# Kernel tuning notes

Hardware: AMD Instinct MI355X
Metric: run time of the kernel (lower is better)

Reference implementation:

```python
import jax, jax.numpy as jnp
import numpy as np

DIM = 2048
N_HEADS = 16
N_KV_HEADS = 4
HEAD_DIM = DIM // N_HEADS


def setup_inputs() -> dict:
    key = jax.random.key(0)
    k1, k2, k3, k4, k5 = jax.random.split(key, 5)
    B, T = 2, 2048
    scale = 1.0 / np.sqrt(DIM)
    x = jax.random.normal(k1, (B, T, DIM), dtype=jnp.float32)
    # weights stored as [in, out] so forward is x @ W (same math as nn.Linear)
    Wq = jax.random.normal(k2, (DIM, DIM), dtype=jnp.float32) * scale
    Wk = jax.random.normal(k3, (DIM, N_KV_HEADS * HEAD_DIM), dtype=jnp.float32) * scale
    Wv = jax.random.normal(k4, (DIM, N_KV_HEADS * HEAD_DIM), dtype=jnp.float32) * scale
    Wo = jax.random.normal(k5, (DIM, DIM), dtype=jnp.float32) * scale
    return {"x": x, "Wq": Wq, "Wk": Wk, "Wv": Wv, "Wo": Wo}


def reference(x, Wq, Wk, Wv, Wo):
    B, T, C = x.shape
    G = N_HEADS // N_KV_HEADS  # query heads per kv head
    # projections
    q = (x @ Wq).reshape(B, T, N_KV_HEADS, G, HEAD_DIM)   # [B,T,K,G,d]
    k = (x @ Wk).reshape(B, T, N_KV_HEADS, HEAD_DIM)      # [B,T,K,d]
    v = (x @ Wv).reshape(B, T, N_KV_HEADS, HEAD_DIM)      # [B,T,K,d]
    # attention scores: grouped heads share kv head (no repeat_interleave copy)
    att = jnp.einsum('btkgd,bskd->bkgts', q, k) / np.sqrt(HEAD_DIM)  # [B,K,G,T,T]
    att = jax.nn.softmax(att, axis=-1)
    out = jnp.einsum('bkgts,bskd->btkgd', att, v).reshape(B, T, C)
    return out @ Wo
```

## Files before the change

kernel.cpp:

```cpp
#include <hip/hip_runtime.h>
#include <hip/hip_bf16.h>

typedef __hip_bfloat16 bf16;
typedef __attribute__((ext_vector_type(8))) short short8;
typedef __attribute__((ext_vector_type(4))) short short4v;
typedef __attribute__((ext_vector_type(4))) float f32x4;

#define DIMC 2048
#define TSEQ 2048
#define NB 2
#define KVH 4
#define NH 16
#define HD 128
#define KVD 512
#define QSCALE 0.12751744f

#if __has_builtin(__builtin_amdgcn_exp2f)
#define EXP2(x) __builtin_amdgcn_exp2f(x)
#else
#define EXP2(x) exp2f(x)
#endif

__device__ __forceinline__ float fmax3(float a, float b, float c) {
  return fmaxf(fmaxf(a, b), c);
}

__device__ __forceinline__ void mfma16(f32x4& acc, short8 a, short8 b) {
  acc = __builtin_amdgcn_mfma_f32_16x16x32_bf16(a, b, acc, 0, 0, 0);
}

__device__ __forceinline__ void gload_lds16(const bf16* g, bf16* l) {
  __builtin_amdgcn_global_load_lds(
      (const __attribute__((address_space(1))) void*)g,
      (__attribute__((address_space(3))) void*)l, 16, 0, 0);
}

__device__ __forceinline__ int swz(int row, int col) {
  return col ^ ((row & 7) << 3);
}

__global__ __launch_bounds__(256) void transpose_all(const float* __restrict__ Wq,
                                                     const float* __restrict__ Wk,
                                                     const float* __restrict__ Wv,
                                                     const float* __restrict__ Wo,
                                                     const float* __restrict__ x,
                                                     bf16* __restrict__ WT3,
                                                     bf16* __restrict__ WoT,
                                                     bf16* __restrict__ xb) {
  const int y = blockIdx.y;
  if (y >= 80) {
    long base = (((long)(y - 80) * 32 + blockIdx.x) * 2048) + threadIdx.x;
#pragma unroll
    for (int j = 0; j < 8; ++j) {
      long i = base + j * 256;
      const f32x4 v = *(const f32x4*)(x + i * 4);
      union { short4v s; bf16 h[4]; } u;
#pragma unroll
      for (int k = 0; k < 4; ++k) u.h[k] = __float2bfloat16(v[k]);
      *(short4v*)(xb + i * 4) = u.s;
    }
    return;
  }
  __shared__ bf16 tile[64][72];
  const float* in;
  bf16* out;
  int C, rb, cb;
  float scale = 1.0f;
  if (y < 32) {
    in = Wq; out = WT3; C = 2048;
    rb = y * 64; cb = blockIdx.x * 64; scale = QSCALE;
  } else if (y < 40) {
    in = Wk; out = WT3 + (long)2048 * DIMC; C = 512;
    rb = blockIdx.x * 64; cb = (y - 32) * 64;
  } else if (y < 48) {
    in = Wv; out = WT3 + (long)2560 * DIMC; C = 512;
    rb = blockIdx.x * 64; cb = (y - 40) * 64;
  } else {
    in = Wo; out = WoT; C = 2048;
    rb = (y - 48) * 64; cb = blockIdx.x * 64;
  }
  int tx = threadIdx.x & 63, ty = threadIdx.x >> 6;
  for (int i = ty; i < 64; i += 4)
    tile[i][tx] = __float2bfloat16(in[(long)(rb + i) * C + cb + tx] * scale);
  __syncthreads();
  for (int i = ty; i < 64; i += 4)
    out[(long)(cb + i) * DIMC + rb + tx] = tile[tx][i];
}

#define XCD_REMAP(NX)                                                          \
  const int flat_ = blockIdx.y * (NX) + blockIdx.x;                            \
  const int tot_ = (NX) * gridDim.y;                                           \
  const int log_ = (flat_ & 7) * (tot_ >> 3) + (flat_ >> 3);                   \
  const long m0 = (long)(log_ / (NX)) * 128, n0 = (long)(log_ % (NX)) * 128;

#define GEMM_BODY(A_, Bt_, K_)                                                  \
  const int tid = threadIdx.x;                                                  \
  const int lane = tid & 63, wid = tid >> 6;                                    \
  const int wm = (wid >> 1) * 64, wn = (wid & 1) * 64;                          \
  f32x4 acc[4][4] = {};                                                         \
  const int srow = lane >> 2, scol = (lane & 3) * 8;                            \
  const bf16* Ag = A_ + (m0 + srow) * (long)K_ + scol;                          \
  const bf16* Bg = Bt_ + (n0 + srow) * (long)K_ + scol;                         \
  for (int k0 = 0; k0 < K_; k0 += 32) {                                         \
    for (int p = 0; p < 2; ++p) {                                               \
      int rr = p * 64 + wid * 16;                                               \
      gload_lds16(Ag + (long)rr * K_ + k0, As + rr * 32);                       \
      gload_lds16(Bg + (long)rr * K_ + k0, Bs + rr * 32);                       \
    }                                                                           \
    __syncthreads();                                                            \
    const int ko = (lane >> 4) * 8;                                             \
    short8 af[4], bq[4];                                                        \
    _Pragma("unroll") for (int i = 0; i < 4; ++i) {                             \
      af[i] = *(const short8*)(As + (wm + i * 16 + (lane & 15)) * 32 + ko);     \
      bq[i] = *(const short8*)(Bs + (wn + i * 16 + (lane & 15)) * 32 + ko);     \
    }                                                                           \
    _Pragma("unroll") for (int i = 0; i < 4; ++i)                               \
      _Pragma("unroll") for (int j = 0; j < 4; ++j)                             \
        mfma16(acc[i][j], af[i], bq[j]);                                        \
    __syncthreads();                                                            \
  }                                                                             \
  const int cr = (lane >> 4) * 4, cc = lane & 15;

__global__ __launch_bounds__(256) void gemm_qkv(const bf16* __restrict__ A,
                                                const bf16* __restrict__ Bt,
                                                bf16* __restrict__ qp,
                                                bf16* __restrict__ kp,
                                                bf16* __restrict__ vT) {
  __shared__ bf16 As[128 * 32];
  __shared__ bf16 Bs[128 * 32];
  XCD_REMAP(24)
  GEMM_BODY(A, Bt, 2048)
#pragma unroll
  for (int i = 0; i < 4; ++i)
#pragma unroll
    for (int j = 0; j < 4; ++j)
#pragma unroll
      for (int r = 0; r < 4; ++r) {
        long m = m0 + wm + i * 16 + cr + r;
        long n = n0 + wn + j * 16 + cc;
        float val = acc[i][j][r];
        if (n0 < 2048) {
          qp[m * DIMC + n] = __float2bfloat16(val);
        } else if (n0 < 2560) {
          kp[m * KVD + (n - 2048)] = __float2bfloat16(val);
        } else {
          long nn = n - 2560;
          long z = (m >> 11) * 4 + (nn >> 7);
          vT[z * (HD * (long)TSEQ) + (nn & 127) * (long)TSEQ + (m & 2047)] =
              __float2bfloat16(val);
        }
      }
}

__global__ __launch_bounds__(256) void gemm_out(const bf16* __restrict__ A,
                                                const bf16* __restrict__ Bt,
                                                float* __restrict__ C) {
  __shared__ bf16 As[128 * 32];
  __shared__ bf16 Bs[128 * 32];
  XCD_REMAP(16)
  GEMM_BODY(A, Bt, 2048)
#pragma unroll
  for (int i = 0; i < 4; ++i)
#pragma unroll
    for (int j = 0; j < 4; ++j)
#pragma unroll
      for (int r = 0; r < 4; ++r) {
        long m = m0 + wm + i * 16 + cr + r;
        long n = n0 + wn + j * 16 + cc;
        C[m * DIMC + n] = acc[i][j][r];
      }
}

__global__ __launch_bounds__(256, 2) void attn_fwd(const bf16* __restrict__ Qp,
                                                   const bf16* __restrict__ Kp,
                                                   const bf16* __restrict__ Vt,
                                                   bf16* __restrict__ AO) {
  __shared__ bf16 Ks[2][64 * 128];
  __shared__ bf16 Vts[2][128 * 64];
  const int tid = threadIdx.x;
  const int lane = tid & 63, wid = tid >> 6;
  const int h = blockIdx.y, b = blockIdx.z;
  const int kv = h >> 2;
  const int t0 = blockIdx.x * 128;
  const int lr = lane & 15, lg = lane >> 4;

  short8 aq[2][4];
#pragma unroll
  for (int f = 0; f < 2; ++f) {
    const bf16* qrow =
        Qp + ((long)(b * TSEQ + t0 + wid * 32 + f * 16 + lr)) * DIMC + h * HD + lg * 8;
#pragma unroll
    for (int c = 0; c < 4; ++c) aq[f][c] = *(const short8*)(qrow + c * 32);
  }
  f32x4 o[2][8] = {};
  float mrun[2] = {-1e30f, -1e30f}, lrun[2] = {0.f, 0.f};

  const bf16* Kg = Kp + (long)b * TSEQ * KVD + kv * HD;
  const bf16* Vg = Vt + ((long)(b * KVH + kv)) * HD * TSEQ;

  const int krow = tid >> 2;
  const int vrow = tid >> 1;
  short8 kreg[2][2], vreg[2][2];
#pragma unroll
  for (int s = 0; s < 2; ++s)
#pragma unroll
    for (int p = 0; p < 2; ++p) {
      kreg[s][p] = *(const short8*)(Kg + (long)krow * KVD + (2 * (tid & 3) + s) * 16 + p * 8);
      vreg[s][p] = *(const short8*)(Vg + (long)vrow * TSEQ + (2 * (tid & 1) + s) * 16 + 8 * p);
    }

  for (int s0 = 0; s0 < TSEQ; s0 += 64) {
    const int buf = (s0 >> 6) & 1;
    bf16* Kb = Ks[buf];
    bf16* Vb = Vts[buf];
#pragma unroll
    for (int s = 0; s < 2; ++s)
#pragma unroll
      for (int p = 0; p < 2; ++p) {
        int kc0 = (2 * (tid & 3) + s) * 16;
        *(short8*)(Kb + krow * 128 + swz(krow, kc0 + p * 8)) = kreg[s][p];
        int va = 2 * (tid & 1) + s;
        union { short8 v8; short4v q[2]; } u;
        u.v8 = vreg[s][p];
        int sl1 = (4 * (va >> 1) + 2 * p + vrow) & 7;
        int sl2 = (4 * (va >> 1) + 2 * p + 1 + vrow) & 7;
        int hf = (va & 1) * 4;
        *(short4v*)(Vb + vrow * 64 + sl1 * 8 + hf) = u.q[0];
        *(short4v*)(Vb + vrow * 64 + sl2 * 8 + hf) = u.q[1];
      }
    __syncthreads();
    if (s0 + 64 < TSEQ) {
#pragma unroll
      for (int s = 0; s < 2; ++s)
#pragma unroll
        for (int p = 0; p < 2; ++p) {
          kreg[s][p] = *(const short8*)(Kg + (long)(s0 + 64 + krow) * KVD +
                                        (2 * (tid & 3) + s) * 16 + p * 8);
          vreg[s][p] = *(const short8*)(Vg + (long)vrow * TSEQ + s0 + 64 +
                                        (2 * (tid & 1) + s) * 16 + 8 * p);
        }
    }

    f32x4 sacc[2][4] = {};
    __builtin_amdgcn_s_setprio(1);
#pragma unroll
    for (int sf = 0; sf < 4; ++sf)
#pragma unroll
      for (int c = 0; c < 4; ++c) {
        int row = sf * 16 + lr;
        short8 kf = *(const short8*)(Kb + row * 128 + swz(row, c * 32 + lg * 8));
        mfma16(sacc[0][sf], kf, aq[0][c]);
        mfma16(sacc[1][sf], kf, aq[1][c]);
      }
    __builtin_amdgcn_s_setprio(0);

    union { short8 s; bf16 h[8]; } pb[2][2];
#pragma unroll
    for (int f = 0; f < 2; ++f) {
      float tmax = fmaxf(sacc[f][0][0], sacc[f][0][1]);
      tmax = fmax3(tmax, sacc[f][0][2], sacc[f][0][3]);
      tmax = fmax3(tmax, sacc[f][1][0], sacc[f][1][1]);
      tmax = fmax3(tmax, sacc[f][1][2], sacc[f][1][3]);
      tmax = fmax3(tmax, sacc[f][2][0], sacc[f][2][1]);
      tmax = fmax3(tmax, sacc[f][2][2], sacc[f][2][3]);
      tmax = fmax3(tmax, sacc[f][3][0], sacc[f][3][1]);
      tmax = fmax3(tmax, sacc[f][3][2], sacc[f][3][3]);
      tmax = fmaxf(tmax, __shfl_xor(tmax, 16));
      tmax = fmaxf(tmax, __shfl_xor(tmax, 32));
      if (__any(tmax > mrun[f] + 8.0f)) {
        float mnew = fmaxf(mrun[f], tmax);
        float fac = EXP2(mrun[f] - mnew);
        mrun[f] = mnew;
        lrun[f] *= fac;
#pragma unroll
        for (int df = 0; df < 8; ++df) o[f][df] *= fac;
      }
      float p4[4][4];
      float ps = 0.f;
#pragma unroll
      for (int sf = 0; sf < 4; ++sf)
#pragma unroll
        for (int r = 0; r < 4; ++r) {
          float pv = EXP2(sacc[f][sf][r] - mrun[f]);
          p4[sf][r] = pv;
          ps += pv;
        }
      lrun[f] += ps;
#pragma unroll
      for (int c2 = 0; c2 < 2; ++c2)
#pragma unroll
        for (int r = 0; r < 4; ++r) {
          pb[f][c2].h[r] = __float2bfloat16(p4[2 * c2][r]);
          pb[f][c2].h[4 + r] = __float2bfloat16(p4[2 * c2 + 1][r]);
        }
    }

    __builtin_amdgcn_s_setprio(1);
#pragma unroll
    for (int c2 = 0; c2 < 2; ++c2) {
#pragma unroll
      for (int df = 0; df < 8; ++df) {
        int row = df * 16 + lr;
        short8 vf = *(const short8*)(Vb + row * 64 + ((4 * c2 + lg + row) & 7) * 8);
        mfma16(o[0][df], vf, pb[0][c2].s);
        mfma16(o[1][df], vf, pb[1][c2].s);
      }
    }
    __builtin_amdgcn_s_setprio(0);
  }

#pragma unroll
  for (int f = 0; f < 2; ++f) {
    lrun[f] += __shfl_xor(lrun[f], 16);
    lrun[f] += __shfl_xor(lrun[f], 32);
  }

#pragma unroll
  for (int f = 0; f < 2; ++f) {
    float inv = 1.0f / lrun[f];
    bf16* obase =
        AO + ((long)(b * TSEQ + t0 + wid * 32 + f * 16 + lr)) * DIMC + h * HD + lg * 4;
#pragma unroll
    for (int df = 0; df < 8; ++df) {
      union { short4v s; bf16 h[4]; } ov;
#pragma unroll
      for (int r = 0; r < 4; ++r) ov.h[r] = __float2bfloat16(o[f][df][r] * inv);
      *(short4v*)(obase + df * 16) = ov.s;
    }
  }
}

extern "C" void kernel_launch(void* const* d_in, const int* in_sizes, int n_in,
                              void* d_out, int out_size, void* d_ws, size_t ws_size,
                              hipStream_t stream) {
  const float* x  = (const float*)d_in[0];
  const float* Wq = (const float*)d_in[1];
  const float* Wk = (const float*)d_in[2];
  const float* Wv = (const float*)d_in[3];
  const float* Wo = (const float*)d_in[4];
  float* out = (float*)d_out;
  bf16* ws = (bf16*)d_ws;

  bf16* xb  = ws;
  bf16* WT3 = xb + 8388608;
  bf16* WoT = WT3 + 6291456;
  bf16* qp  = WoT + 4194304;
  bf16* kp  = qp + 8388608;
  bf16* vT  = kp + 2097152;

  transpose_all<<<dim3(32, 112), 256, 0, stream>>>(Wq, Wk, Wv, Wo, x, WT3, WoT, xb);

  gemm_qkv<<<dim3(24, 32), 256, 0, stream>>>(xb, WT3, qp, kp, vT);

  bf16* ao = xb;
  attn_fwd<<<dim3(16, 16, 2), 256, 0, stream>>>(qp, kp, vT, ao);

  gemm_out<<<dim3(16, 32), 256, 0, stream>>>(ao, WoT, out);
}
```

Before: 219.2 us.

## Use 128-key single-buffered LDS tiles in attention with trailing barrier

The attention kernel now processes 128 keys per iteration instead of 64, using a single LDS buffer for K and V^T (same total LDS) rather than double buffering, and adds a second barrier at the end of each iteration. This halves the number of loop iterations, barriers per key and online-softmax rescale checks. The cost is more registers (sacc doubles, prefetch registers double) and the loss of LDS double buffering, which may reduce occupancy or overlap.

```diff
diff --git a/kernel.cpp b/kernel.cpp
--- a/kernel.cpp
+++ b/kernel.cpp
@@ -175,8 +175,8 @@
                                                    const bf16* __restrict__ Kp,
                                                    const bf16* __restrict__ Vt,
                                                    bf16* __restrict__ AO) {
-  __shared__ bf16 Ks[2][64 * 128];
-  __shared__ bf16 Vts[2][128 * 64];
+  __shared__ bf16 Ks[128 * 128];
+  __shared__ bf16 Vts[128 * 128];
   const int tid = threadIdx.x;
   const int lane = tid & 63, wid = tid >> 6;
   const int h = blockIdx.y, b = blockIdx.z;
@@ -198,73 +198,59 @@
   const bf16* Kg = Kp + (long)b * TSEQ * KVD + kv * HD;
   const bf16* Vg = Vt + ((long)(b * KVH + kv)) * HD * TSEQ;
 
-  const int krow = tid >> 2;
-  const int vrow = tid >> 1;
-  short8 kreg[2][2], vreg[2][2];
-#pragma unroll
-  for (int s = 0; s < 2; ++s)
-#pragma unroll
-    for (int p = 0; p < 2; ++p) {
-      kreg[s][p] = *(const short8*)(Kg + (long)krow * KVD + (2 * (tid & 3) + s) * 16 + p * 8);
-      vreg[s][p] = *(const short8*)(Vg + (long)vrow * TSEQ + (2 * (tid & 1) + s) * 16 + 8 * p);
-    }
-
-  for (int s0 = 0; s0 < TSEQ; s0 += 64) {
-    const int buf = (s0 >> 6) & 1;
-    bf16* Kb = Ks[buf];
-    bf16* Vb = Vts[buf];
-#pragma unroll
-    for (int s = 0; s < 2; ++s)
-#pragma unroll
-      for (int p = 0; p < 2; ++p) {
-        int kc0 = (2 * (tid & 3) + s) * 16;
-        *(short8*)(Kb + krow * 128 + swz(krow, kc0 + p * 8)) = kreg[s][p];
-        int va = 2 * (tid & 1) + s;
-        union { short8 v8; short4v q[2]; } u;
-        u.v8 = vreg[s][p];
-        int sl1 = (4 * (va >> 1) + 2 * p + vrow) & 7;
-        int sl2 = (4 * (va >> 1) + 2 * p + 1 + vrow) & 7;
-        int hf = (va & 1) * 4;
-        *(short4v*)(Vb + vrow * 64 + sl1 * 8 + hf) = u.q[0];
-        *(short4v*)(Vb + vrow * 64 + sl2 * 8 + hf) = u.q[1];
-      }
+  const int kr = tid >> 1, kh = (tid & 1) * 64;
+  short8 kreg[8], vreg[8];
+#pragma unroll
+  for (int p = 0; p < 8; ++p) {
+    kreg[p] = *(const short8*)(Kg + (long)kr * KVD + kh + 8 * p);
+    vreg[p] = *(const short8*)(Vg + (long)kr * TSEQ + kh + 8 * p);
+  }
+
+  for (int s0 = 0; s0 < TSEQ; s0 += 128) {
+#pragma unroll
+    for (int p = 0; p < 8; ++p) {
+      *(short8*)(Ks + kr * 128 + swz(kr, kh + 8 * p)) = kreg[p];
+      int S0 = kh + 8 * p;
+      int t = S0 >> 4, lg0 = (S0 >> 2) & 3;
+      union { short8 v8; short4v q[2]; } u;
+      u.v8 = vreg[p];
+      int base4 = 4 * (t >> 1);
+      int sl1 = (base4 + lg0 + kr) & 15;
+      int sl2 = (base4 + lg0 + 1 + kr) & 15;
+      int hf = (t & 1) * 4;
+      *(short4v*)(Vts + kr * 128 + sl1 * 8 + hf) = u.q[0];
+      *(short4v*)(Vts + kr * 128 + sl2 * 8 + hf) = u.q[1];
+    }
     __syncthreads();
-    if (s0 + 64 < TSEQ) {
-#pragma unroll
-      for (int s = 0; s < 2; ++s)
-#pragma unroll
-        for (int p = 0; p < 2; ++p) {
-          kreg[s][p] = *(const short8*)(Kg + (long)(s0 + 64 + krow) * KVD +
-                                        (2 * (tid & 3) + s) * 16 + p * 8);
-          vreg[s][p] = *(const short8*)(Vg + (long)vrow * TSEQ + s0 + 64 +
-                                        (2 * (tid & 1) + s) * 16 + 8 * p);
-        }
-    }
-
-    f32x4 sacc[2][4] = {};
+    if (s0 + 128 < TSEQ) {
+#pragma unroll
+      for (int p = 0; p < 8; ++p) {
+        kreg[p] = *(const short8*)(Kg + (long)(s0 + 128 + kr) * KVD + kh + 8 * p);
+        vreg[p] = *(const short8*)(Vg + (long)kr * TSEQ + s0 + 128 + kh + 8 * p);
+      }
+    }
+
+    f32x4 sacc[2][8] = {};
     __builtin_amdgcn_s_setprio(1);
 #pragma unroll
-    for (int sf = 0; sf < 4; ++sf)
+    for (int sf = 0; sf < 8; ++sf)
 #pragma unroll
       for (int c = 0; c < 4; ++c) {
         int row = sf * 16 + lr;
-        short8 kf = *(const short8*)(Kb + row * 128 + swz(row, c * 32 + lg * 8));
+        short8 kf = *(const short8*)(Ks + row * 128 + swz(row, c * 32 + lg * 8));
         mfma16(sacc[0][sf], kf, aq[0][c]);
         mfma16(sacc[1][sf], kf, aq[1][c]);
       }
     __builtin_amdgcn_s_setprio(0);
 
-    union { short8 s; bf16 h[8]; } pb[2][2];
+    union { short8 s; bf16 h[8]; } pb[2][4];
 #pragma unroll
     for (int f = 0; f < 2; ++f) {
-      float tmax = fmaxf(sacc[f][0][0], sacc[f][0][1]);
-      tmax = fmax3(tmax, sacc[f][0][2], sacc[f][0][3]);
-      tmax = fmax3(tmax, sacc[f][1][0], sacc[f][1][1]);
-      tmax = fmax3(tmax, sacc[f][1][2], sacc[f][1][3]);
-      tmax = fmax3(tmax, sacc[f][2][0], sacc[f][2][1]);
-      tmax = fmax3(tmax, sacc[f][2][2], sacc[f][2][3]);
-      tmax = fmax3(tmax, sacc[f][3][0], sacc[f][3][1]);
-      tmax = fmax3(tmax, sacc[f][3][2], sacc[f][3][3]);
+      float tmax = sacc[f][0][0];
+#pragma unroll
+      for (int sf = 0; sf < 8; ++sf)
+#pragma unroll
+        for (int r = 0; r < 4; ++r) tmax = fmaxf(tmax, sacc[f][sf][r]);
       tmax = fmaxf(tmax, __shfl_xor(tmax, 16));
       tmax = fmaxf(tmax, __shfl_xor(tmax, 32));
       if (__any(tmax > mrun[f] + 8.0f)) {
@@ -275,38 +261,33 @@
 #pragma unroll
         for (int df = 0; df < 8; ++df) o[f][df] *= fac;
       }
-      float p4[4][4];
       float ps = 0.f;
 #pragma unroll
-      for (int sf = 0; sf < 4; ++sf)
+      for (int c2 = 0; c2 < 4; ++c2)
 #pragma unroll
         for (int r = 0; r < 4; ++r) {
-          float pv = EXP2(sacc[f][sf][r] - mrun[f]);
-          p4[sf][r] = pv;
-          ps += pv;
+          float v0 = EXP2(sacc[f][2 * c2][r] - mrun[f]);
+          float v1 = EXP2(sacc[f][2 * c2 + 1][r] - mrun[f]);
+          ps += v0 + v1;
+          pb[f][c2].h[r] = __float2bfloat16(v0);
+          pb[f][c2].h[4 + r] = __float2bfloat16(v1);
         }
       lrun[f] += ps;
-#pragma unroll
-      for (int c2 = 0; c2 < 2; ++c2)
-#pragma unroll
-        for (int r = 0; r < 4; ++r) {
-          pb[f][c2].h[r] = __float2bfloat16(p4[2 * c2][r]);
-          pb[f][c2].h[4 + r] = __float2bfloat16(p4[2 * c2 + 1][r]);
-        }
     }
 
     __builtin_amdgcn_s_setprio(1);
 #pragma unroll
-    for (int c2 = 0; c2 < 2; ++c2) {
+    for (int c2 = 0; c2 < 4; ++c2) {
 #pragma unroll
       for (int df = 0; df < 8; ++df) {
         int row = df * 16 + lr;
-        short8 vf = *(const short8*)(Vb + row * 64 + ((4 * c2 + lg + row) & 7) * 8);
+        short8 vf = *(const short8*)(Vts + row * 128 + ((4 * c2 + lg + row) & 15) * 8);
         mfma16(o[0][df], vf, pb[0][c2].s);
         mfma16(o[1][df], vf, pb[1][c2].s);
       }
     }
     __builtin_amdgcn_s_setprio(0);
+    __syncthreads();
   }
 
 #pragma unroll
```

Measured after the change: 279.6 us. 27.5% more time.
